# Kernel optimization log

Measured on AMD Instinct MI355X. Metric: run time of the kernel, lower is better.

Reference implementation:

```python
import jax, jax.numpy as jnp
import numpy as np

N_SRC = 50000
N_DST = 50000
N_EDGES = 1600000
BATCH = 64


def setup_inputs() -> dict:
    key = jax.random.key(0)
    k1, k2, k3, k4, k5 = jax.random.split(key, 5)
    x = jax.random.normal(k1, (BATCH, N_SRC), dtype=jnp.float32)
    # per-edge scalar weights, init like Synapse.init_weight: U(-v, v), v = sqrt(1/fan_in)~sqrt(1/32)
    v = float(np.sqrt(1.0 / 32.0))
    k = jax.random.uniform(k2, (N_EDGES,), dtype=jnp.float32, minval=-v, maxval=v)
    b = jax.random.normal(k3, (N_DST,), dtype=jnp.float32) * 0.1
    edge_src = jax.random.randint(k4, (N_EDGES,), 0, N_SRC, dtype=jnp.int32)
    edge_dst = jax.random.randint(k5, (N_EDGES,), 0, N_DST, dtype=jnp.int32)
    return {"x": x, "k": k, "b": b, "edge_src": edge_src, "edge_dst": edge_dst}


def reference(x, k, b, edge_src, edge_dst):
    # Synapse: out_e = k_e * source_output  (source output is x[:, src(e)], shape [batch])
    # msgs: [n_edges, batch]
    msgs = x.T[edge_src] * k[:, None]
    # DestinationNeuron: sum of dendrite outputs per destination + bias
    agg = jax.ops.segment_sum(msgs, edge_dst, num_segments=N_DST)  # [n_dst, batch]
    out = jax.nn.relu(agg.T + b[None, :])  # [batch, n_dst]
    return out
```

## Files before the change

### kernel.cpp

```cpp
#include <hip/hip_runtime.h>
#include <hip/hip_bf16.h>
#include <stdint.h>

#define N_SRC 50000
#define N_DST 50000
#define N_EDGES 1600000
#define BATCH 64

#define DPB 32
#define NBUCK ((N_DST + DPB - 1) / DPB)
#define CAPB 1344
#define EPB 6400
#define PBLOCKS ((N_EDGES + EPB - 1) / EPB)
#define TBLOCKS ((N_SRC + 63) / 64)
#define PTHREADS 1024
#define GTHREADS 512
#define NT ((EPB + PTHREADS - 1) / PTHREADS)

__global__ __launch_bounds__(PTHREADS) void fused_tp_kernel(
        const float* __restrict__ x,
        __hip_bfloat16* __restrict__ xTb,
        const float* __restrict__ k,
        const int* __restrict__ esrc,
        const int* __restrict__ edst,
        int* __restrict__ gcur,
        uint64_t* __restrict__ part) {
    __shared__ int bcnt[NBUCK];
    __shared__ int bcur[NBUCK];
    __shared__ float tile[64][65];

    if (blockIdx.x < PBLOCKS) {
        const int e0 = blockIdx.x * EPB;
        const int n = min(EPB, N_EDGES - e0);

        for (int i = threadIdx.x; i < NBUCK; i += PTHREADS) bcnt[i] = 0;
        __syncthreads();

        int dreg[NT];
#pragma unroll
        for (int t = 0; t < NT; ++t) {
            const int i = t * PTHREADS + threadIdx.x;
            dreg[t] = (i < n) ? edst[e0 + i] : -1;
            if (dreg[t] >= 0) atomicAdd(&bcnt[dreg[t] >> 5], 1);
        }
        __syncthreads();

        for (int bi = threadIdx.x; bi < NBUCK; bi += PTHREADS) {
            const int c = bcnt[bi];
            bcur[bi] = c ? atomicAdd(&gcur[bi], c) : 0;
        }
        __syncthreads();

#pragma unroll
        for (int t = 0; t < NT; ++t) {
            const int i = t * PTHREADS + threadIdx.x;
            if (dreg[t] >= 0) {
                const int e = e0 + i;
                const int d = dreg[t];
                const int bkt = d >> 5;
                const int slot = atomicAdd(&bcur[bkt], 1);
                if (slot < CAPB) {
                    const uint32_t lo = (uint32_t)esrc[e] |
                                        ((uint32_t)(d & 31) << 16);
                    part[(size_t)bkt * CAPB + slot] =
                        (uint64_t)lo | ((uint64_t)__float_as_uint(k[e]) << 32);
                }
            }
        }
    } else {
        const int s0 = (blockIdx.x - PBLOCKS) * 64;
        const int tid = threadIdx.x;

#pragma unroll
        for (int it = 0; it < 4; ++it) {
            const int i = it * 1024 + tid;
            const int bi = i >> 6;
            const int sc = i & 63;
            const int s = s0 + sc;
            float v = 0.0f;
            if (s < N_SRC) v = x[(size_t)bi * N_SRC + s];
            tile[bi][sc] = v;
        }
        __syncthreads();
#pragma unroll
        for (int it = 0; it < 4; ++it) {
            const int i = it * 1024 + tid;
            const int sc = i >> 6;
            const int bi = i & 63;
            const int s = s0 + sc;
            if (s < N_SRC)
                xTb[(size_t)s * 64 + bi] = __float2bfloat16(tile[bi][sc]);
        }
    }
}

__global__ __launch_bounds__(GTHREADS, 8) void gather_kernel(
        const __hip_bfloat16* __restrict__ xTb,
        const int* __restrict__ gcur,
        const uint64_t* __restrict__ part,
        const float* __restrict__ b,
        float* __restrict__ out) {
    __shared__ uint64_t raw[CAPB];
    __shared__ uint64_t sorted[CAPB];
    __shared__ int dbase[DPB + 1];
    __shared__ int dcur[DPB];

    const uint2* __restrict__ xTu2 = (const uint2*)xTb;

    const int bk = blockIdx.x;
    const size_t base = (size_t)bk * CAPB;
    const int n = min(gcur[bk], CAPB);
    const int d0 = bk * DPB;
    const int tid = threadIdx.x;
    const int wid = tid >> 6;
    const int lane = tid & 63;
    const int rp = lane >> 4;
    const int m = lane & 15;

    if (tid < DPB) dcur[tid] = 0;
    __syncthreads();

    for (int i = tid; i < n; i += GTHREADS) {
        const uint64_t r = part[base + i];
        raw[i] = r;
        atomicAdd(&dcur[(int)((r >> 16) & 31)], 1);
    }
    __syncthreads();

    if (wid == 0) {
        const int orig = (lane < DPB) ? dcur[lane] : 0;
        int v = orig;
#pragma unroll
        for (int d = 1; d < DPB; d <<= 1) {
            const int t = __shfl_up(v, d, 64);
            if (lane >= d) v += t;
        }
        if (lane < DPB) dbase[lane] = v - orig;
        if (lane == DPB - 1) dbase[DPB] = v;
    }
    __syncthreads();
    if (tid < DPB) dcur[tid] = dbase[tid];
    __syncthreads();

    for (int i = tid; i < n; i += GTHREADS) {
        const uint64_t r = raw[i];
        const int p = atomicAdd(&dcur[(int)((r >> 16) & 31)], 1);
        sorted[p] = r;
    }
    __syncthreads();

    float acc[4][4];
    const int dlo = wid * 4;
#pragma unroll
    for (int q = 0; q < 4; ++q) {
        const int dl = dlo + q;
        float a0 = 0.0f, a1 = 0.0f, a2 = 0.0f, a3 = 0.0f;
        int j = dbase[dl];
        const int je = dbase[dl + 1];
        for (; j + 8 <= je; j += 8) {
            const uint64_t r0 = sorted[j + rp];
            const uint64_t r1 = sorted[j + 4 + rp];
            const uint2 x0 = xTu2[(size_t)((uint32_t)r0 & 0xFFFFu) * 16 + m];
            const uint2 x1 = xTu2[(size_t)((uint32_t)r1 & 0xFFFFu) * 16 + m];
            const float k0 = __uint_as_float((uint32_t)(r0 >> 32));
            const float k1 = __uint_as_float((uint32_t)(r1 >> 32));
            a0 = fmaf(k0, __uint_as_float(x0.x << 16), a0);
            a1 = fmaf(k0, __uint_as_float(x0.x & 0xFFFF0000u), a1);
            a2 = fmaf(k0, __uint_as_float(x0.y << 16), a2);
            a3 = fmaf(k0, __uint_as_float(x0.y & 0xFFFF0000u), a3);
            a0 = fmaf(k1, __uint_as_float(x1.x << 16), a0);
            a1 = fmaf(k1, __uint_as_float(x1.x & 0xFFFF0000u), a1);
            a2 = fmaf(k1, __uint_as_float(x1.y << 16), a2);
            a3 = fmaf(k1, __uint_as_float(x1.y & 0xFFFF0000u), a3);
        }
        for (; j < je; j += 4) {
            const int idx = j + rp;
            const bool v = idx < je;
            const uint64_t r = sorted[v ? idx : j];
            const float kv = v ? __uint_as_float((uint32_t)(r >> 32)) : 0.0f;
            const uint2 xv = xTu2[(size_t)((uint32_t)r & 0xFFFFu) * 16 + m];
            a0 = fmaf(kv, __uint_as_float(xv.x << 16), a0);
            a1 = fmaf(kv, __uint_as_float(xv.x & 0xFFFF0000u), a1);
            a2 = fmaf(kv, __uint_as_float(xv.y << 16), a2);
            a3 = fmaf(kv, __uint_as_float(xv.y & 0xFFFF0000u), a3);
        }
        a0 += __shfl_xor(a0, 16); a0 += __shfl_xor(a0, 32);
        a1 += __shfl_xor(a1, 16); a1 += __shfl_xor(a1, 32);
        a2 += __shfl_xor(a2, 16); a2 += __shfl_xor(a2, 32);
        a3 += __shfl_xor(a3, 16); a3 += __shfl_xor(a3, 32);
        acc[q][0] = a0; acc[q][1] = a1; acc[q][2] = a2; acc[q][3] = a3;
    }
    __syncthreads();

    float* stg = (float*)sorted;
    if (rp == 0) {
#pragma unroll
        for (int q = 0; q < 4; ++q) {
            const int dl = dlo + q;
            stg[dl * 65 + 4 * m + 0] = acc[q][0];
            stg[dl * 65 + 4 * m + 1] = acc[q][1];
            stg[dl * 65 + 4 * m + 2] = acc[q][2];
            stg[dl * 65 + 4 * m + 3] = acc[q][3];
        }
    }
    __syncthreads();

    for (int i = tid; i < 64 * DPB; i += GTHREADS) {
        const int dl = i & (DPB - 1);
        const int bi = i >> 5;
        const int d = d0 + dl;
        if (d < N_DST)
            out[(size_t)bi * N_DST + d] = fmaxf(stg[dl * 65 + bi] + b[d], 0.0f);
    }
}

__global__ void transpose_only_kernel(const float* __restrict__ x,
                                      __hip_bfloat16* __restrict__ xTb) {
    __shared__ float tile[64][65];
    const int s0 = blockIdx.x * 64;
    const int tid = threadIdx.x;
#pragma unroll
    for (int it = 0; it < 16; ++it) {
        const int i = it * 256 + tid;
        const int bi = i >> 6;
        const int sc = i & 63;
        const int s = s0 + sc;
        float v = 0.0f;
        if (s < N_SRC) v = x[(size_t)bi * N_SRC + s];
        tile[bi][sc] = v;
    }
    __syncthreads();
#pragma unroll
    for (int it = 0; it < 16; ++it) {
        const int i = it * 256 + tid;
        const int sc = i >> 6;
        const int bi = i & 63;
        const int s = s0 + sc;
        if (s < N_SRC) xTb[(size_t)s * 64 + bi] = __float2bfloat16(tile[bi][sc]);
    }
}

__global__ void scatter_kernel(const __hip_bfloat16* __restrict__ xTb,
                               const float* __restrict__ k,
                               const int* __restrict__ esrc,
                               const int* __restrict__ edst,
                               float* __restrict__ agg) {
    const int gtid = blockIdx.x * blockDim.x + threadIdx.x;
    const int wid = gtid >> 6;
    const int lane = threadIdx.x & 63;
    const int nwaves = (gridDim.x * blockDim.x) >> 6;
    for (int e = wid; e < N_EDGES; e += nwaves) {
        atomicAdd(&agg[(size_t)edst[e] * 64 + lane],
                  k[e] * __bfloat162float(xTb[(size_t)esrc[e] * 64 + lane]));
    }
}

__global__ void finish_kernel(const float* __restrict__ agg,
                              const float* __restrict__ b,
                              float* __restrict__ out) {
    __shared__ float tile[64 * 65];
    const int d0 = blockIdx.x * 64;
    const int tid = threadIdx.x;
#pragma unroll
    for (int it = 0; it < 16; ++it) {
        const int i = it * 256 + tid;
        const int dl = i >> 6;
        const int bi = i & 63;
        const int d = d0 + dl;
        float v = 0.0f;
        if (d < N_DST) v = agg[(size_t)d * 64 + bi];
        tile[bi * 65 + dl] = v;
    }
    __syncthreads();
#pragma unroll
    for (int it = 0; it < 16; ++it) {
        const int i = it * 256 + tid;
        const int bi = i >> 6;
        const int dl = i & 63;
        const int d = d0 + dl;
        if (d < N_DST)
            out[(size_t)bi * N_DST + d] = fmaxf(tile[bi * 65 + dl] + b[d], 0.0f);
    }
}

extern "C" void kernel_launch(void* const* d_in, const int* in_sizes, int n_in,
                              void* d_out, int out_size, void* d_ws, size_t ws_size,
                              hipStream_t stream) {
    const float* x    = (const float*)d_in[0];
    const float* k    = (const float*)d_in[1];
    const float* b    = (const float*)d_in[2];
    const int*   esrc = (const int*)d_in[3];
    const int*   edst = (const int*)d_in[4];
    float* out = (float*)d_out;

    const size_t xt_bytes   = (size_t)N_SRC * 64 * sizeof(__hip_bfloat16);
    const size_t part_bytes = (size_t)NBUCK * CAPB * sizeof(uint64_t);
    const size_t off_gcur   = xt_bytes + part_bytes;
    const size_t need_new   = off_gcur + ((NBUCK * 4 + 4095) & ~4095ull);

    __hip_bfloat16* xTb = (__hip_bfloat16*)d_ws;

    if (ws_size >= need_new) {
        uint64_t* part = (uint64_t*)((char*)d_ws + xt_bytes);
        int* gcur      = (int*)((char*)d_ws + off_gcur);

        hipMemsetAsync(gcur, 0, NBUCK * sizeof(int), stream);
        fused_tp_kernel<<<PBLOCKS + TBLOCKS, PTHREADS, 0, stream>>>(
            x, xTb, k, esrc, edst, gcur, part);
        gather_kernel<<<NBUCK, GTHREADS, 0, stream>>>(xTb, gcur, part, b, out);
    } else {
        transpose_only_kernel<<<TBLOCKS, 256, 0, stream>>>(x, xTb);
        float* agg = (float*)((char*)d_ws + ((xt_bytes + 255) & ~255ull));
        hipMemsetAsync(agg, 0, (size_t)N_DST * 64 * sizeof(float), stream);
        scatter_kernel<<<2048, 256, 0, stream>>>(xTb, k, esrc, edst, agg);
        const int nblk_f = (N_DST + 63) / 64;
        finish_kernel<<<nblk_f, 256, 0, stream>>>(agg, b, out);
    }
}
```

Measured before the change: 69.97 us.

## Stage bucketed edge records in LDS via prefix scan before global write

The partition phase now computes an exclusive prefix scan of per-bucket counts with wavefront shuffles, then places each edge record into a shared-memory staging array ordered by bucket. A second pass copies the staged records to their global bucket slots, so neighbouring threads write neighbouring addresses within each bucket run instead of scattering 8-byte stores. This costs more LDS, since the partition union is now around 70KB, plus extra scan passes and barriers, which may lower occupancy. The record now stores the full destination index in its upper 16 bits instead of only the low 5 bits.

```diff
diff --git a/kernel.cpp b/kernel.cpp
--- a/kernel.cpp
+++ b/kernel.cpp
@@ -9,6 +9,7 @@
 
 #define DPB 32
 #define NBUCK ((N_DST + DPB - 1) / DPB)
+#define NCHUNK ((NBUCK + 63) / 64)
 #define CAPB 1344
 #define EPB 6400
 #define PBLOCKS ((N_EDGES + EPB - 1) / EPB)
@@ -25,13 +26,25 @@
         const int* __restrict__ edst,
         int* __restrict__ gcur,
         uint64_t* __restrict__ part) {
-    __shared__ int bcnt[NBUCK];
-    __shared__ int bcur[NBUCK];
-    __shared__ float tile[64][65];
+    __shared__ union SM {
+        struct {
+            uint64_t recs[EPB];
+            int bcnt[NBUCK];
+            int bbase[NBUCK];
+            int gbase[NBUCK];
+            int csum[32];
+        } p;
+        float tile[64][65];
+    } sm;
 
     if (blockIdx.x < PBLOCKS) {
+        int* bcnt = sm.p.bcnt;
+        int* bbase = sm.p.bbase;
+        int* gbase = sm.p.gbase;
         const int e0 = blockIdx.x * EPB;
         const int n = min(EPB, N_EDGES - e0);
+        const int lane = threadIdx.x & 63;
+        const int w = threadIdx.x >> 6;
 
         for (int i = threadIdx.x; i < NBUCK; i += PTHREADS) bcnt[i] = 0;
         __syncthreads();
@@ -45,27 +58,60 @@
         }
         __syncthreads();
 
-        for (int bi = threadIdx.x; bi < NBUCK; bi += PTHREADS) {
-            const int c = bcnt[bi];
-            bcur[bi] = c ? atomicAdd(&gcur[bi], c) : 0;
+        for (int c = w; c < NCHUNK; c += 16) {
+            const int i = c * 64 + lane;
+            const int orig = (i < NBUCK) ? bcnt[i] : 0;
+            int v = orig;
+#pragma unroll
+            for (int dd = 1; dd < 64; dd <<= 1) {
+                const int t = __shfl_up(v, dd, 64);
+                if (lane >= dd) v += t;
+            }
+            if (i < NBUCK) bbase[i] = v - orig;
+            if (lane == 63) sm.p.csum[c] = v;
+        }
+        __syncthreads();
+        if (w == 0) {
+            const int orig = (lane < NCHUNK) ? sm.p.csum[lane] : 0;
+            int v = orig;
+#pragma unroll
+            for (int dd = 1; dd < 64; dd <<= 1) {
+                const int t = __shfl_up(v, dd, 64);
+                if (lane >= dd) v += t;
+            }
+            if (lane < NCHUNK) sm.p.csum[lane] = v - orig;
+        }
+        __syncthreads();
+
+        for (int i = threadIdx.x; i < NBUCK; i += PTHREADS) {
+            const int ex = bbase[i] + sm.p.csum[i >> 6];
+            const int c = bcnt[i];
+            bbase[i] = ex;
+            gbase[i] = i * CAPB + (c ? atomicAdd(&gcur[i], c) : 0);
+            bcnt[i] = ex;
         }
         __syncthreads();
 
 #pragma unroll
         for (int t = 0; t < NT; ++t) {
-            const int i = t * PTHREADS + threadIdx.x;
             if (dreg[t] >= 0) {
+                const int i = t * PTHREADS + threadIdx.x;
                 const int e = e0 + i;
                 const int d = dreg[t];
-                const int bkt = d >> 5;
-                const int slot = atomicAdd(&bcur[bkt], 1);
-                if (slot < CAPB) {
-                    const uint32_t lo = (uint32_t)esrc[e] |
-                                        ((uint32_t)(d & 31) << 16);
-                    part[(size_t)bkt * CAPB + slot] =
-                        (uint64_t)lo | ((uint64_t)__float_as_uint(k[e]) << 32);
-                }
+                const int lpos = atomicAdd(&bcnt[d >> 5], 1);
+                const uint32_t lo = (uint32_t)esrc[e] | ((uint32_t)d << 16);
+                sm.p.recs[lpos] =
+                    (uint64_t)lo | ((uint64_t)__float_as_uint(k[e]) << 32);
             }
+        }
+        __syncthreads();
+
+        for (int i = threadIdx.x; i < n; i += PTHREADS) {
+            const uint64_t r = sm.p.recs[i];
+            const int d = (int)((r >> 16) & 0xFFFFu);
+            const int bkt = d >> 5;
+            const int gslot = gbase[bkt] + (i - bbase[bkt]);
+            if (gslot < (bkt + 1) * CAPB) part[gslot] = r;
         }
     } else {
         const int s0 = (blockIdx.x - PBLOCKS) * 64;
@@ -79,7 +125,7 @@
             const int s = s0 + sc;
             float v = 0.0f;
             if (s < N_SRC) v = x[(size_t)bi * N_SRC + s];
-            tile[bi][sc] = v;
+            sm.tile[bi][sc] = v;
         }
         __syncthreads();
 #pragma unroll
@@ -89,7 +135,7 @@
             const int bi = i & 63;
             const int s = s0 + sc;
             if (s < N_SRC)
-                xTb[(size_t)s * 64 + bi] = __float2bfloat16(tile[bi][sc]);
+                xTb[(size_t)s * 64 + bi] = __float2bfloat16(sm.tile[bi][sc]);
         }
     }
 }
```

Result: faster. 61.84 us (-11.6%).
